# Performance work log

Hardware: AMD Instinct MI355X
Metric: run time of the kernel (lower is better)

The kernel has to match this reference:

```python
import jax, jax.numpy as jnp
import numpy as np

B, C, W, H = 4, 256, 64, 64

def setup_inputs() -> dict:
    key = jax.random.key(0)
    ks = jax.random.split(key, 6)
    return {
        "fm_source": jax.random.normal(ks[0], (B, C, W, H), dtype=jnp.float32),
        "fm_reference": jax.random.normal(ks[1], (B, C, W, H), dtype=jnp.float32),
        "w_lambda": jax.random.normal(ks[2], (1, C, 1, 1), dtype=jnp.float32) * 0.05,
        "b_lambda": jax.random.normal(ks[3], (1,), dtype=jnp.float32) * 0.05,
        "w_beta": jax.random.normal(ks[4], (1, C, 1, 1), dtype=jnp.float32) * 0.05,
        "b_beta": jax.random.normal(ks[5], (1,), dtype=jnp.float32) * 0.05,
    }

def reference(fm_source, fm_reference, w_lambda, b_lambda, w_beta, b_beta):
    b, c, w, h = fm_reference.shape
    n = w * h
    # 1x1 convs on the reference feature map -> per-pixel scalars, flattened to [B, N]
    wl = w_lambda.reshape(c)
    wb = w_beta.reshape(c)
    ref_flat = fm_reference.reshape(b, c, n)   # [B, C, N]
    src_flat = fm_source.reshape(b, c, n)      # [B, C, N]
    old_lambda = jnp.einsum("bcn,c->bn", ref_flat, wl) + b_lambda[0]  # [B, N]
    old_beta = jnp.einsum("bcn,c->bn", ref_flat, wb) + b_beta[0]      # [B, N]
    # energy[b, i, j] = <src pixel i, ref pixel j> over channels
    energy = jnp.einsum("bci,bcj->bij", src_flat, ref_flat)  # [B, N, N]
    attention = jax.nn.softmax(energy, axis=-1)              # softmax over ref pixels j
    # new_lambda[b, i] = sum_j old_lambda[b, j] * attention[b, i, j]
    new_lambda = jnp.einsum("bj,bij->bi", old_lambda, attention).reshape(b, 1, w, h)
    new_beta = jnp.einsum("bj,bij->bi", old_beta, attention).reshape(b, 1, w, h)
    # broadcast modulation over the 256 channels
    return new_lambda * fm_source + new_beta
```

## Files before the change

kernel.cpp:

```cpp
#include <hip/hip_runtime.h>


#define B_ 4
#define C_ 256
#define N_ 4096
#define LOG2E 1.44269504f
#define SHIFT2 86.5617f
#define JSLICE 8
#define BN_ (B_ * N_)
#define NT_ 16

typedef _Float16 half_t;
typedef _Float16 v8h  __attribute__((ext_vector_type(8)));
typedef _Float16 v4h  __attribute__((ext_vector_type(4)));
typedef float    v16f __attribute__((ext_vector_type(16)));

#define GLDS16(g, l) __builtin_amdgcn_global_load_lds(                         \
    (const __attribute__((address_space(1))) void*)(g),                        \
    (__attribute__((address_space(3))) void*)(l), 16, 0, 0)

__global__ void k_prep(const float* __restrict__ src,
                       const float* __restrict__ ref,
                       const float* __restrict__ wl, const float* __restrict__ bl,
                       const float* __restrict__ wb, const float* __restrict__ bb,
                       half_t* __restrict__ s16, half_t* __restrict__ r16,
                       float* __restrict__ oldL, float* __restrict__ oldB) {
    if (blockIdx.z == 8) {
        int b  = blockIdx.y;
        int n0 = blockIdx.x * 64;
        int nl = threadIdx.x & 63;
        int cq = threadIdx.x >> 6;
        const float* p = ref + ((size_t)b * C_ + cq * 64) * N_ + n0 + nl;
        float aL = 0.f, aB = 0.f;
#pragma unroll 8
        for (int c = 0; c < 64; c++) {
            float v = p[(size_t)c * N_];
            aL += v * wl[cq * 64 + c];
            aB += v * wb[cq * 64 + c];
        }
        __shared__ float red[8][64];
        red[cq][nl]     = aL;
        red[4 + cq][nl] = aB;
        __syncthreads();
        if (threadIdx.x < 64) {
            int t = threadIdx.x;
            oldL[(size_t)b * N_ + n0 + t] =
                red[0][t] + red[1][t] + red[2][t] + red[3][t] + bl[0];
        } else if (threadIdx.x < 128) {
            int t = threadIdx.x - 64;
            oldB[(size_t)b * N_ + n0 + t] =
                red[4][t] + red[5][t] + red[6][t] + red[7][t] + bb[0];
        }
        return;
    }
    __shared__ float tile[64][65];
    int z  = blockIdx.z;
    int b  = z & 3;
    const float* in  = (z < B_) ? src : ref;
    half_t*      out = (z < B_) ? s16 : r16;
    float scale      = (z < B_) ? LOG2E : 1.0f;
    int c0 = blockIdx.y * 64;
    int n0 = blockIdx.x * 64;
    int tx = threadIdx.x & 15, ty = threadIdx.x >> 4;
#pragma unroll
    for (int q = 0; q < 4; q++) {
        int c = ty + q * 16;
        float4 v = *(const float4*)(in + ((size_t)b * C_ + c0 + c) * N_ + n0 + tx * 4);
        tile[c][tx * 4 + 0] = v.x;
        tile[c][tx * 4 + 1] = v.y;
        tile[c][tx * 4 + 2] = v.z;
        tile[c][tx * 4 + 3] = v.w;
    }
    __syncthreads();
    int r   = threadIdx.x & 31;
    int lhi = (threadIdx.x >> 5) & 1;
    int wv  = threadIdx.x >> 6;
#pragma unroll
    for (int nt = 0; nt < 2; nt++) {
        int nl = nt * 32 + r;
        v8h o;
#pragma unroll
        for (int e = 0; e < 8; e++)
            o[e] = (half_t)(tile[wv * 16 + lhi * 8 + e][nl] * scale);
        size_t tj = (size_t)(n0 >> 5) + nt;
        size_t kb = (size_t)(c0 >> 4) + wv;
        *(v8h*)(out + ((((size_t)b * 128 + tj) * 16 + kb) * 64 + (threadIdx.x & 63)) * 8) = o;
    }
}

__global__ __launch_bounds__(512, 2) void k_flash(
        const half_t* __restrict__ sT, const half_t* __restrict__ rT,
        const float* __restrict__ oldL, const float* __restrict__ oldB,
        float* __restrict__ part ) {
    __shared__ half_t lds[2][8192];
    int bid    = blockIdx.x;
    int b      = bid & 3;
    int jslice = (bid >> 2) & (JSLICE - 1);
    int iblock = bid >> 5;
    int tid    = threadIdx.x;
    int wv     = tid >> 6;
    int lane   = tid & 63;
    int l31    = lane & 31, lhi = lane >> 5;
    int ti     = iblock * 8 + wv;
    int i0     = ti * 32;
    int j0     = jslice * (N_ / JSLICE);
    int tj0    = j0 >> 5;

    const half_t* aP = sT + (((size_t)b * 128 + ti) * 16) * 512 + (size_t)lane * 8;
    v8h a[16];
#pragma unroll
    for (int kb = 0; kb < 16; kb++) a[kb] = *(const v8h*)(aP + (size_t)kb * 512);

    const half_t* bBase = rT + (((size_t)b * 128 + tj0) * 16) * 512;
    const float*  oLp = oldL + (size_t)b * N_ + j0 + l31;
    const float*  oBp = oldB + (size_t)b * N_ + j0 + l31;

    float sp[16], sl[16], sb[16];
#pragma unroll
    for (int r = 0; r < 16; r++) { sp[r] = 0.f; sl[r] = 0.f; sb[r] = 0.f; }

#pragma unroll
    for (int q = 0; q < 2; q++) {
        int chunk = q * 8 + wv;
        GLDS16(bBase + (size_t)chunk * 512 + (size_t)lane * 8,
               &lds[0][(size_t)chunk * 512]);
    }

    for (int jt = 0; jt < NT_; jt++) {
        __syncthreads();
        if (jt + 1 < NT_) {
            const half_t* g = bBase + (size_t)(jt + 1) * 8192;
#pragma unroll
            for (int q = 0; q < 2; q++) {
                int chunk = q * 8 + wv;
                GLDS16(g + (size_t)chunk * 512 + (size_t)lane * 8,
                       &lds[(jt + 1) & 1][(size_t)chunk * 512]);
            }
        }
        const half_t* bt = lds[jt & 1] + (size_t)lane * 8;
        v16f acc0, acc1;
#pragma unroll
        for (int r = 0; r < 16; r++) { acc0[r] = -SHIFT2; acc1[r] = 0.f; }
#pragma unroll
        for (int kb = 0; kb < 8; kb++) {
            acc0 = __builtin_amdgcn_mfma_f32_32x32x16_f16(
                a[kb],     *(const v8h*)(bt + (size_t)kb * 512),       acc0, 0, 0, 0);
            acc1 = __builtin_amdgcn_mfma_f32_32x32x16_f16(
                a[kb + 8], *(const v8h*)(bt + (size_t)(kb + 8) * 512), acc1, 0, 0, 0);
        }
        float lam = oLp[jt * 32], bet = oBp[jt * 32];
#pragma unroll
        for (int r = 0; r < 16; r++) {
            float p = __builtin_amdgcn_exp2f(acc0[r] + acc1[r]);
            sp[r] += p;
            sl[r] += p * lam;
            sb[r] += p * bet;
        }
    }

    float* pSP = part + ((size_t)jslice * 3 + 0) * BN_;
    float* pSL = part + ((size_t)jslice * 3 + 1) * BN_;
    float* pSB = part + ((size_t)jslice * 3 + 2) * BN_;
#pragma unroll
    for (int r = 0; r < 16; r++) {
        float tp = sp[r], tl = sl[r], tb = sb[r];
#pragma unroll
        for (int m = 1; m <= 16; m <<= 1) {
            tp += __shfl_xor(tp, m, 64);
            tl += __shfl_xor(tl, m, 64);
            tb += __shfl_xor(tb, m, 64);
        }
        if (l31 == 0) {
            int row = (r & 3) + 8 * (r >> 2) + 4 * lhi;
            size_t ig = (size_t)b * N_ + i0 + row;
            pSP[ig] = tp; pSL[ig] = tl; pSB[ig] = tb;
        }
    }
}

__global__ void k_post(const float* __restrict__ src,
                       const float* __restrict__ part,
                       float* __restrict__ out) {
    int b  = blockIdx.x;
    int n0 = blockIdx.y * 1024;
    int c0 = blockIdx.z * 16;
    int t  = threadIdx.x;
    size_t bn = (size_t)b * N_ + n0 + t * 4;
    float4 sp = {0.f, 0.f, 0.f, 0.f}, sl = sp, sb = sp;
#pragma unroll
    for (int s = 0; s < JSLICE; s++) {
        float4 p0 = *(const float4*)(part + ((size_t)s * 3 + 0) * BN_ + bn);
        float4 p1 = *(const float4*)(part + ((size_t)s * 3 + 1) * BN_ + bn);
        float4 p2 = *(const float4*)(part + ((size_t)s * 3 + 2) * BN_ + bn);
        sp.x += p0.x; sp.y += p0.y; sp.z += p0.z; sp.w += p0.w;
        sl.x += p1.x; sl.y += p1.y; sl.z += p1.z; sl.w += p1.w;
        sb.x += p2.x; sb.y += p2.y; sb.z += p2.z; sb.w += p2.w;
    }
    float4 L, T;
    L.x = sl.x / sp.x; L.y = sl.y / sp.y; L.z = sl.z / sp.z; L.w = sl.w / sp.w;
    T.x = sb.x / sp.x; T.y = sb.y / sp.y; T.z = sb.z / sp.z; T.w = sb.w / sp.w;
    const float* sp0 = src + ((size_t)b * C_ + c0) * N_ + n0 + t * 4;
    float*       op0 = out + ((size_t)b * C_ + c0) * N_ + n0 + t * 4;
#pragma unroll 4
    for (int c = 0; c < 16; c++) {
        float4 v = *(const float4*)(sp0 + (size_t)c * N_);
        float4 o;
        o.x = L.x * v.x + T.x;
        o.y = L.y * v.y + T.y;
        o.z = L.z * v.z + T.z;
        o.w = L.w * v.w + T.w;
        *(float4*)(op0 + (size_t)c * N_) = o;
    }
}

extern "C" void kernel_launch(void* const* d_in, const int* in_sizes, int n_in,
                              void* d_out, int out_size, void* d_ws, size_t ws_size,
                              hipStream_t stream) {
    const float* src = (const float*)d_in[0];
    const float* ref = (const float*)d_in[1];
    const float* wl  = (const float*)d_in[2];
    const float* bl  = (const float*)d_in[3];
    const float* wb  = (const float*)d_in[4];
    const float* bb  = (const float*)d_in[5];
    float* out = (float*)d_out;

    float* oldL = (float*)d_ws;
    float* oldB = oldL + BN_;
    float* part = oldB + BN_;
    size_t needF  = ((size_t)2 + 3 * JSLICE) * BN_ * sizeof(float);
    size_t need16 = (size_t)2 * B_ * N_ * C_ * sizeof(half_t);
    half_t* s16;
    if (ws_size >= needF + need16) s16 = (half_t*)((char*)d_ws + needF);
    else                           s16 = (half_t*)d_out;
    half_t* r16 = s16 + (size_t)B_ * N_ * C_;

    k_prep<<<dim3(N_ / 64, C_ / 64, 9), 256, 0, stream>>>(
        src, ref, wl, bl, wb, bb, s16, r16, oldL, oldB);
    k_flash<<<512, 512, 0, stream>>>(s16, r16, oldL, oldB, part);
    k_post<<<dim3(B_, N_ / 1024, C_ / 16), 256, 0, stream>>>(src, part, out);
}
```

Baseline: 146.8 us.

## Fuse source conversion into flash kernel and reduce partials via atomics

Drops the separate fp16 conversion of the source map: the flash kernel now loads fp32 source columns directly, scales them by log2(e) and converts them into its A-fragment registers. The lambda/beta 1x1 conv is merged into the reference transpose kernel, with per-channel-block partial sums combined through atomicAdd into memset-zeroed buffers. The flash kernel is restructured to 4 j-slices with 4x larger LDS phases (64 KB double buffer), and it reduces across slices with atomics instead of writing per-slice partials. These cut workspace traffic and one kernel pass. The costs are a memset, strided uncoalesced fp32 A loads, and higher LDS use that may limit occupancy.

```diff
diff --git a/kernel.cpp b/kernel.cpp
--- a/kernel.cpp
+++ b/kernel.cpp
@@ -6,97 +6,88 @@
 #define N_ 4096
 #define LOG2E 1.44269504f
 #define SHIFT2 86.5617f
-#define JSLICE 8
+#define JSLICE 4
 #define BN_ (B_ * N_)
-#define NT_ 16
+#define NT_ 32
+#define PH_ 8
 
 typedef _Float16 half_t;
 typedef _Float16 v8h  __attribute__((ext_vector_type(8)));
-typedef _Float16 v4h  __attribute__((ext_vector_type(4)));
 typedef float    v16f __attribute__((ext_vector_type(16)));
 
 #define GLDS16(g, l) __builtin_amdgcn_global_load_lds(                         \
     (const __attribute__((address_space(1))) void*)(g),                        \
     (__attribute__((address_space(3))) void*)(l), 16, 0, 0)
 
-__global__ void k_prep(const float* __restrict__ src,
-                       const float* __restrict__ ref,
-                       const float* __restrict__ wl, const float* __restrict__ bl,
-                       const float* __restrict__ wb, const float* __restrict__ bb,
-                       half_t* __restrict__ s16, half_t* __restrict__ r16,
+__global__ void k_prep(const float* __restrict__ ref,
+                       const float* __restrict__ wl,
+                       const float* __restrict__ wb,
+                       half_t* __restrict__ r16,
                        float* __restrict__ oldL, float* __restrict__ oldB) {
-    if (blockIdx.z == 8) {
-        int b  = blockIdx.y;
-        int n0 = blockIdx.x * 64;
-        int nl = threadIdx.x & 63;
-        int cq = threadIdx.x >> 6;
-        const float* p = ref + ((size_t)b * C_ + cq * 64) * N_ + n0 + nl;
-        float aL = 0.f, aB = 0.f;
-#pragma unroll 8
-        for (int c = 0; c < 64; c++) {
-            float v = p[(size_t)c * N_];
-            aL += v * wl[cq * 64 + c];
-            aB += v * wb[cq * 64 + c];
-        }
-        __shared__ float red[8][64];
-        red[cq][nl]     = aL;
-        red[4 + cq][nl] = aB;
-        __syncthreads();
-        if (threadIdx.x < 64) {
-            int t = threadIdx.x;
-            oldL[(size_t)b * N_ + n0 + t] =
-                red[0][t] + red[1][t] + red[2][t] + red[3][t] + bl[0];
-        } else if (threadIdx.x < 128) {
-            int t = threadIdx.x - 64;
-            oldB[(size_t)b * N_ + n0 + t] =
-                red[4][t] + red[5][t] + red[6][t] + red[7][t] + bb[0];
-        }
-        return;
-    }
     __shared__ float tile[64][65];
-    int z  = blockIdx.z;
-    int b  = z & 3;
-    const float* in  = (z < B_) ? src : ref;
-    half_t*      out = (z < B_) ? s16 : r16;
-    float scale      = (z < B_) ? LOG2E : 1.0f;
+    __shared__ float red[8][64];
+    int b  = blockIdx.z;
     int c0 = blockIdx.y * 64;
     int n0 = blockIdx.x * 64;
-    int tx = threadIdx.x & 15, ty = threadIdx.x >> 4;
+    int tid = threadIdx.x;
+    int tx = tid & 15, ty = tid >> 4;
 #pragma unroll
     for (int q = 0; q < 4; q++) {
         int c = ty + q * 16;
-        float4 v = *(const float4*)(in + ((size_t)b * C_ + c0 + c) * N_ + n0 + tx * 4);
+        float4 v = *(const float4*)(ref + ((size_t)b * C_ + c0 + c) * N_ + n0 + tx * 4);
         tile[c][tx * 4 + 0] = v.x;
         tile[c][tx * 4 + 1] = v.y;
         tile[c][tx * 4 + 2] = v.z;
         tile[c][tx * 4 + 3] = v.w;
     }
     __syncthreads();
-    int r   = threadIdx.x & 31;
-    int lhi = (threadIdx.x >> 5) & 1;
-    int wv  = threadIdx.x >> 6;
+    int r   = tid & 31;
+    int lhi = (tid >> 5) & 1;
+    int wv  = tid >> 6;
 #pragma unroll
     for (int nt = 0; nt < 2; nt++) {
         int nl = nt * 32 + r;
         v8h o;
 #pragma unroll
         for (int e = 0; e < 8; e++)
-            o[e] = (half_t)(tile[wv * 16 + lhi * 8 + e][nl] * scale);
+            o[e] = (half_t)tile[wv * 16 + lhi * 8 + e][nl];
         size_t tj = (size_t)(n0 >> 5) + nt;
         size_t kb = (size_t)(c0 >> 4) + wv;
-        *(v8h*)(out + ((((size_t)b * 128 + tj) * 16 + kb) * 64 + (threadIdx.x & 63)) * 8) = o;
+        *(v8h*)(r16 + ((((size_t)b * 128 + tj) * 16 + kb) * 64 + (tid & 63)) * 8) = o;
+    }
+    int n  = tid & 63;
+    int cq = tid >> 6;
+    float aL = 0.f, aB = 0.f;
+#pragma unroll
+    for (int c = 0; c < 16; c++) {
+        float v = tile[cq * 16 + c][n];
+        aL += v * wl[c0 + cq * 16 + c];
+        aB += v * wb[c0 + cq * 16 + c];
+    }
+    red[cq][n]     = aL;
+    red[4 + cq][n] = aB;
+    __syncthreads();
+    if (tid < 64) {
+        atomicAdd(&oldL[(size_t)b * N_ + n0 + tid],
+                  red[0][tid] + red[1][tid] + red[2][tid] + red[3][tid]);
+    } else if (tid < 128) {
+        int u = tid - 64;
+        atomicAdd(&oldB[(size_t)b * N_ + n0 + u],
+                  red[4][u] + red[5][u] + red[6][u] + red[7][u]);
     }
 }
 
 __global__ __launch_bounds__(512, 2) void k_flash(
-        const half_t* __restrict__ sT, const half_t* __restrict__ rT,
+        const float* __restrict__ src, const half_t* __restrict__ rT,
         const float* __restrict__ oldL, const float* __restrict__ oldB,
-        float* __restrict__ part ) {
-    __shared__ half_t lds[2][8192];
+        const float* __restrict__ bl, const float* __restrict__ bb,
+        float* __restrict__ sumP, float* __restrict__ sumL,
+        float* __restrict__ sumB) {
+    __shared__ half_t lds[2][32768];
     int bid    = blockIdx.x;
     int b      = bid & 3;
     int jslice = (bid >> 2) & (JSLICE - 1);
-    int iblock = bid >> 5;
+    int iblock = bid >> 4;
     int tid    = threadIdx.x;
     int wv     = tid >> 6;
     int lane   = tid & 63;
@@ -106,61 +97,75 @@
     int j0     = jslice * (N_ / JSLICE);
     int tj0    = j0 >> 5;
 
-    const half_t* aP = sT + (((size_t)b * 128 + ti) * 16) * 512 + (size_t)lane * 8;
+    const float* aS = src + (size_t)b * C_ * N_ + i0 + l31;
     v8h a[16];
 #pragma unroll
-    for (int kb = 0; kb < 16; kb++) a[kb] = *(const v8h*)(aP + (size_t)kb * 512);
+    for (int kb = 0; kb < 16; kb++) {
+        v8h o;
+#pragma unroll
+        for (int e = 0; e < 8; e++)
+            o[e] = (half_t)(aS[(size_t)(kb * 16 + lhi * 8 + e) * N_] * LOG2E);
+        a[kb] = o;
+    }
 
     const half_t* bBase = rT + (((size_t)b * 128 + tj0) * 16) * 512;
     const float*  oLp = oldL + (size_t)b * N_ + j0 + l31;
     const float*  oBp = oldB + (size_t)b * N_ + j0 + l31;
+    float bl0 = bl[0], bb0 = bb[0];
 
     float sp[16], sl[16], sb[16];
 #pragma unroll
     for (int r = 0; r < 16; r++) { sp[r] = 0.f; sl[r] = 0.f; sb[r] = 0.f; }
 
 #pragma unroll
-    for (int q = 0; q < 2; q++) {
+    for (int q = 0; q < 8; q++) {
         int chunk = q * 8 + wv;
         GLDS16(bBase + (size_t)chunk * 512 + (size_t)lane * 8,
                &lds[0][(size_t)chunk * 512]);
     }
 
-    for (int jt = 0; jt < NT_; jt++) {
+    for (int ph = 0; ph < PH_; ph++) {
         __syncthreads();
-        if (jt + 1 < NT_) {
-            const half_t* g = bBase + (size_t)(jt + 1) * 8192;
-#pragma unroll
-            for (int q = 0; q < 2; q++) {
+        if (ph + 1 < PH_) {
+            const half_t* g = bBase + (size_t)(ph + 1) * 32768;
+#pragma unroll
+            for (int q = 0; q < 8; q++) {
                 int chunk = q * 8 + wv;
                 GLDS16(g + (size_t)chunk * 512 + (size_t)lane * 8,
-                       &lds[(jt + 1) & 1][(size_t)chunk * 512]);
+                       &lds[(ph + 1) & 1][(size_t)chunk * 512]);
             }
         }
-        const half_t* bt = lds[jt & 1] + (size_t)lane * 8;
-        v16f acc0, acc1;
-#pragma unroll
-        for (int r = 0; r < 16; r++) { acc0[r] = -SHIFT2; acc1[r] = 0.f; }
-#pragma unroll
-        for (int kb = 0; kb < 8; kb++) {
-            acc0 = __builtin_amdgcn_mfma_f32_32x32x16_f16(
-                a[kb],     *(const v8h*)(bt + (size_t)kb * 512),       acc0, 0, 0, 0);
-            acc1 = __builtin_amdgcn_mfma_f32_32x32x16_f16(
-                a[kb + 8], *(const v8h*)(bt + (size_t)(kb + 8) * 512), acc1, 0, 0, 0);
-        }
-        float lam = oLp[jt * 32], bet = oBp[jt * 32];
-#pragma unroll
-        for (int r = 0; r < 16; r++) {
-            float p = __builtin_amdgcn_exp2f(acc0[r] + acc1[r]);
-            sp[r] += p;
-            sl[r] += p * lam;
-            sb[r] += p * bet;
-        }
-    }
-
-    float* pSP = part + ((size_t)jslice * 3 + 0) * BN_;
-    float* pSL = part + ((size_t)jslice * 3 + 1) * BN_;
-    float* pSB = part + ((size_t)jslice * 3 + 2) * BN_;
+        float lamv[4], betv[4];
+#pragma unroll
+        for (int t = 0; t < 4; t++) {
+            lamv[t] = oLp[(ph * 4 + t) * 32] + bl0;
+            betv[t] = oBp[(ph * 4 + t) * 32] + bb0;
+        }
+        const half_t* btb = lds[ph & 1] + (size_t)lane * 8;
+#pragma unroll
+        for (int t = 0; t < 4; t++) {
+            const half_t* bt = btb + (size_t)t * 8192;
+            v16f acc0, acc1;
+#pragma unroll
+            for (int r = 0; r < 16; r++) { acc0[r] = -SHIFT2; acc1[r] = 0.f; }
+#pragma unroll
+            for (int kb = 0; kb < 8; kb++) {
+                acc0 = __builtin_amdgcn_mfma_f32_32x32x16_f16(
+                    a[kb],     *(const v8h*)(bt + (size_t)kb * 512),       acc0, 0, 0, 0);
+                acc1 = __builtin_amdgcn_mfma_f32_32x32x16_f16(
+                    a[kb + 8], *(const v8h*)(bt + (size_t)(kb + 8) * 512), acc1, 0, 0, 0);
+            }
+            float lam = lamv[t], bet = betv[t];
+#pragma unroll
+            for (int r = 0; r < 16; r++) {
+                float p = __builtin_amdgcn_exp2f(acc0[r] + acc1[r]);
+                sp[r] += p;
+                sl[r] += p * lam;
+                sb[r] += p * bet;
+            }
+        }
+    }
+
 #pragma unroll
     for (int r = 0; r < 16; r++) {
         float tp = sp[r], tl = sl[r], tb = sb[r];
@@ -173,29 +178,26 @@
         if (l31 == 0) {
             int row = (r & 3) + 8 * (r >> 2) + 4 * lhi;
             size_t ig = (size_t)b * N_ + i0 + row;
-            pSP[ig] = tp; pSL[ig] = tl; pSB[ig] = tb;
+            atomicAdd(&sumP[ig], tp);
+            atomicAdd(&sumL[ig], tl);
+            atomicAdd(&sumB[ig], tb);
         }
     }
 }
 
 __global__ void k_post(const float* __restrict__ src,
-                       const float* __restrict__ part,
+                       const float* __restrict__ sumP,
+                       const float* __restrict__ sumL,
+                       const float* __restrict__ sumB,
                        float* __restrict__ out) {
     int b  = blockIdx.x;
     int n0 = blockIdx.y * 1024;
     int c0 = blockIdx.z * 16;
     int t  = threadIdx.x;
     size_t bn = (size_t)b * N_ + n0 + t * 4;
-    float4 sp = {0.f, 0.f, 0.f, 0.f}, sl = sp, sb = sp;
-#pragma unroll
-    for (int s = 0; s < JSLICE; s++) {
-        float4 p0 = *(const float4*)(part + ((size_t)s * 3 + 0) * BN_ + bn);
-        float4 p1 = *(const float4*)(part + ((size_t)s * 3 + 1) * BN_ + bn);
-        float4 p2 = *(const float4*)(part + ((size_t)s * 3 + 2) * BN_ + bn);
-        sp.x += p0.x; sp.y += p0.y; sp.z += p0.z; sp.w += p0.w;
-        sl.x += p1.x; sl.y += p1.y; sl.z += p1.z; sl.w += p1.w;
-        sb.x += p2.x; sb.y += p2.y; sb.z += p2.z; sb.w += p2.w;
-    }
+    float4 sp = *(const float4*)(sumP + bn);
+    float4 sl = *(const float4*)(sumL + bn);
+    float4 sb = *(const float4*)(sumB + bn);
     float4 L, T;
     L.x = sl.x / sp.x; L.y = sl.y / sp.y; L.z = sl.z / sp.z; L.w = sl.w / sp.w;
     T.x = sb.x / sp.x; T.y = sb.y / sp.y; T.z = sb.z / sp.z; T.w = sb.w / sp.w;
@@ -226,16 +228,20 @@
 
     float* oldL = (float*)d_ws;
     float* oldB = oldL + BN_;
-    float* part = oldB + BN_;
-    size_t needF  = ((size_t)2 + 3 * JSLICE) * BN_ * sizeof(float);
-    size_t need16 = (size_t)2 * B_ * N_ * C_ * sizeof(half_t);
-    half_t* s16;
-    if (ws_size >= needF + need16) s16 = (half_t*)((char*)d_ws + needF);
-    else                           s16 = (half_t*)d_out;
-    half_t* r16 = s16 + (size_t)B_ * N_ * C_;
-
-    k_prep<<<dim3(N_ / 64, C_ / 64, 9), 256, 0, stream>>>(
-        src, ref, wl, bl, wb, bb, s16, r16, oldL, oldB);
-    k_flash<<<512, 512, 0, stream>>>(s16, r16, oldL, oldB, part);
-    k_post<<<dim3(B_, N_ / 1024, C_ / 16), 256, 0, stream>>>(src, part, out);
-}
+    float* sumP = oldB + BN_;
+    float* sumL = sumP + BN_;
+    float* sumB = sumL + BN_;
+    size_t needF  = (size_t)5 * BN_ * sizeof(float);
+    size_t need16 = (size_t)B_ * N_ * C_ * sizeof(half_t);
+    half_t* r16;
+    if (ws_size >= needF + need16) r16 = (half_t*)((char*)d_ws + needF);
+    else                           r16 = (half_t*)d_out;
+
+    hipMemsetAsync(d_ws, 0, needF, stream);
+    k_prep<<<dim3(N_ / 64, C_ / 64, B_), 256, 0, stream>>>(
+        ref, wl, wb, r16, oldL, oldB);
+    k_flash<<<B_ * JSLICE * 16, 512, 0, stream>>>(
+        src, r16, oldL, oldB, bl, bb, sumP, sumL, sumB);
+    k_post<<<dim3(B_, N_ / 1024, C_ / 16), 256, 0, stream>>>(
+        src, sumP, sumL, sumB, out);
+}
```

Measured after the change: 145.8 us. Within noise of the previous version (-0.7%).
